# Performance work log

Measured on AMD Instinct MI355X. Metric: run time of the kernel, lower is better.

## Reference

```python
import jax, jax.numpy as jnp
import numpy as np

WIN = 7
K1 = 0.01
K2 = 0.03
COV_NORM = WIN * WIN / (WIN * WIN - 1.0)  # unbiased covariance correction


def _box_filter(t):
    # t: [B, 1, H, W]; valid conv with uniform 7x7 window (mean filter)
    w = jnp.ones((1, 1, WIN, WIN), t.dtype) / (WIN * WIN)
    return jax.lax.conv_general_dilated(
        t, w, window_strides=(1, 1), padding='VALID',
        dimension_numbers=('NCHW', 'OIHW', 'NCHW'))


def setup_inputs() -> dict:
    key = jax.random.key(0)
    kx, ky = jax.random.split(key)
    B, C, H, W = 64, 1, 384, 384
    X = jax.random.normal(kx, (B, C, H, W), dtype=jnp.float32)
    Y = jax.random.normal(ky, (B, C, H, W), dtype=jnp.float32)
    data_range = jnp.ones((B,), dtype=jnp.float32)
    return {"X": X, "Y": Y, "data_range": data_range}


def reference(X, Y, data_range):
    ux = _box_filter(X)
    uy = _box_filter(Y)
    uxx = _box_filter(X * X)
    uxy = _box_filter(X * Y)
    uyy = _box_filter(Y * Y)

    vx = COV_NORM * (uxx - ux * ux)
    vy = COV_NORM * (uyy - uy * uy)
    vxy = COV_NORM * (uxy - ux * uy)

    L = data_range.reshape(-1, 1, 1, 1)  # per-sample dynamic range
    C1 = (K1 * L) ** 2
    C2 = (K2 * L) ** 2

    N1 = 2.0 * ux * uy + C1
    N2 = 2.0 * vxy + C2
    D1 = ux * ux + uy * uy + C1
    D2 = vx + vy + C2
    S = (N1 * N2) / (D1 * D2)

    # original: mean SSIM per sample, then mean over batch; equal-size maps so
    # this equals the mean over the per-sample means
    per_sample = jnp.mean(S, axis=(1, 2, 3))
    return 1.0 - jnp.mean(per_sample)
```

## Files before the change

kernel.cpp:

```cpp
#include <hip/hip_runtime.h>

#define IMH 384
#define IMW 384
#define OH 378
#define OW 378
#define NB 64
#define SROWS 21
#define INROWS 27
#define NSTRIP 18
#define BLOCK 256
#define GSTRIDE 26
#define RING 6


template <int CTRL>
__device__ __forceinline__ float dpp_sh(float v) {
    return __int_as_float(__builtin_amdgcn_update_dpp(
        0, __float_as_int(v), CTRL, 0xf, 0xf, true));
}

__device__ __forceinline__ float2 f2add(float2 a, float2 b) { return make_float2(a.x + b.x, a.y + b.y); }
__device__ __forceinline__ float2 f2sub(float2 a, float2 b) { return make_float2(a.x - b.x, a.y - b.y); }
__device__ __forceinline__ float2 f2mul(float2 a, float2 b) { return make_float2(a.x * b.x, a.y * b.y); }
__device__ __forceinline__ float2 f2fma(float2 a, float2 b, float2 c) {
    return make_float2(fmaf(a.x, b.x, c.x), fmaf(a.y, b.y, c.y));
}
__device__ __forceinline__ float2 f2fnma(float2 a, float2 b, float2 c) {
    return make_float2(fmaf(-a.x, b.x, c.x), fmaf(-a.y, b.y, c.y));
}
__device__ __forceinline__ float2 f2fms(float2 a, float s, float2 c) {
    return make_float2(fmaf(a.x, s, -c.x), fmaf(a.y, s, -c.y));
}
__device__ __forceinline__ float2 f2s(float s) { return make_float2(s, s); }

__global__ __launch_bounds__(BLOCK)
__attribute__((amdgpu_waves_per_eu(5, 8)))
void ssim_kernel(
    const float* __restrict__ X, const float* __restrict__ Y,
    const float* __restrict__ data_range, float* __restrict__ partials)
{
    const int tid   = threadIdx.x;
    const int g     = tid >> 4;
    const int j     = tid & 15;
    const int strip = blockIdx.x;
    const int b     = blockIdx.y;
    const int y0    = strip * SROWS;

    const float* __restrict__ Xb = X + b * (IMH * IMW);
    const float* __restrict__ Yb = Y + b * (IMH * IMW);

    __shared__ float sX[RING][IMW];
    __shared__ float sY[RING][IMW];

    const bool stg = (tid < 192);
    const int  sc  = ((tid < 96) ? tid : tid - 96) * 4;
    const float* __restrict__ gp =
        ((tid < 96) ? Xb : Yb) + y0 * IMW + sc;
    float* const sbase = (tid < 96) ? &sX[0][0] : &sY[0][0];

    const int ce  = g * GSTRIDE + 2 * j;
    const int cin = min(ce, IMW - 2);
    const float2 vmask = make_float2(
        ((j <= 12) && (ce     < OW)) ? 1.f : 0.f,
        ((j <= 12) && (ce + 1 < OW)) ? 1.f : 0.f);

    const float L     = data_range[b];
    const float C1    = (0.01f * L) * (0.01f * L);
    const float C2    = (0.03f * L) * (0.03f * L);
    const float inv49 = 1.0f / 49.0f;
    const float covn  = 49.0f / 48.0f;

    if (stg) {
        #pragma unroll
        for (int k = 0; k < 5; ++k) {
            const float4 v = *(const float4*)(gp + k * IMW);
            *(float4*)(sbase + k * IMW + sc) = v;
        }
    }
    float4 gb0, gb1, gb2;
    if (stg) {
        gb0 = *(const float4*)(gp + 5 * IMW);
        gb1 = *(const float4*)(gp + 6 * IMW);
        gb2 = *(const float4*)(gp + 7 * IMW);
    }
    __syncthreads();

    float2 xh[7], yh[7];
    #pragma unroll
    for (int k = 0; k < 7; ++k) { xh[k] = f2s(0.f); yh[k] = f2s(0.f); }
    float2 V0 = f2s(0.f), V1 = f2s(0.f), V2 = f2s(0.f),
           V3 = f2s(0.f), V4 = f2s(0.f);
    float2 ls2 = f2s(0.f);

    #pragma unroll
    for (int r = 0; r < INROWS; ++r) {
        if (r + 5 < INROWS) {
            if (stg) {
                const float4 v = (r % 3 == 0) ? gb0 : (r % 3 == 1) ? gb1 : gb2;
                *(float4*)(sbase + ((r + 5) % RING) * IMW + sc) = v;
            }
        }
        if (r + 8 < INROWS) {
            if (stg) {
                const float4 v = *(const float4*)(gp + (r + 8) * IMW);
                if (r % 3 == 0) gb0 = v; else if (r % 3 == 1) gb1 = v; else gb2 = v;
            }
        }

        const float2 x = *(const float2*)&sX[r % RING][cin];
        const float2 y = *(const float2*)&sY[r % RING][cin];

        const int ks = r % 7;
        const float2 xo = xh[ks], yo = yh[ks];
        V0 = f2add(V0, f2sub(x, xo));
        V1 = f2add(V1, f2sub(y, yo));
        V2 = f2fma(x, x, V2);  V2 = f2fnma(xo, xo, V2);
        V3 = f2fma(x, y, V3);  V3 = f2fnma(xo, yo, V3);
        V4 = f2fma(y, y, V4);  V4 = f2fnma(yo, yo, V4);
        xh[ks] = x; yh[ks] = y;

        if (r >= 6) {
            const float2 Vv[5] = {V0, V1, V2, V3, V4};
            float Se[5], So[5];
            #pragma unroll
            for (int p = 0; p < 5; ++p) {
                const float e  = Vv[p].x;
                const float o  = Vv[p].y;
                const float pp = e + o;
                float B = pp + dpp_sh<0x101>(pp);
                float C = B + dpp_sh<0x102>(B);
                Se[p] = C - dpp_sh<0x103>(o);
                So[p] = C - e;
            }
            const float2 S0 = make_float2(Se[0], So[0]);
            const float2 S1 = make_float2(Se[1], So[1]);
            const float2 S2 = make_float2(Se[2], So[2]);
            const float2 S3 = make_float2(Se[3], So[3]);
            const float2 S4 = make_float2(Se[4], So[4]);

            float2 ux   = f2mul(S0, f2s(inv49));
            float2 uy   = f2mul(S1, f2s(inv49));
            float2 uxux = f2mul(ux, ux);
            float2 uyuy = f2mul(uy, uy);
            float2 uxuy = f2mul(ux, uy);
            float2 vx   = f2mul(f2fms(S2, inv49, uxux), f2s(covn));
            float2 vy   = f2mul(f2fms(S4, inv49, uyuy), f2s(covn));
            float2 vxy  = f2mul(f2fms(S3, inv49, uxuy), f2s(covn));
            float2 N1   = f2fma(f2s(2.f), uxuy, f2s(C1));
            float2 N2   = f2fma(f2s(2.f), vxy, f2s(C2));
            float2 D1   = f2add(f2add(uxux, uyuy), f2s(C1));
            float2 D2   = f2add(f2add(vx, vy), f2s(C2));
            float2 num  = f2mul(N1, N2);
            float2 den  = f2mul(D1, D2);
            const float rdd = __builtin_amdgcn_rcpf(den.x * den.y);
            float2 s2 = make_float2(num.x * den.y * rdd,
                                    num.y * den.x * rdd);
            ls2 = f2fma(s2, vmask, ls2);
        }

        __syncthreads();
    }

    float lsum = ls2.x + ls2.y;
    __shared__ float red[BLOCK / 64];
    #pragma unroll
    for (int off = 32; off > 0; off >>= 1)
        lsum += __shfl_down(lsum, off, 64);
    if ((tid & 63) == 0) red[tid >> 6] = lsum;
    __syncthreads();
    if (tid == 0) {
        float bs = 0.f;
        #pragma unroll
        for (int k = 0; k < BLOCK / 64; ++k) bs += red[k];
        partials[b * NSTRIP + strip] = bs;
    }
}

__global__ void finalize_kernel(const float* __restrict__ partials,
                                float* __restrict__ out)
{
    float v = 0.f;
    #pragma unroll
    for (int k = 0; k < NSTRIP; ++k)
        v += partials[threadIdx.x + 64 * k];
    #pragma unroll
    for (int off = 32; off > 0; off >>= 1)
        v += __shfl_down(v, off, 64);
    if (threadIdx.x == 0)
        out[0] = 1.0f - v * (1.0f / (float)(NB * OH * OW));
}

extern "C" void kernel_launch(void* const* d_in, const int* in_sizes, int n_in,
                              void* d_out, int out_size, void* d_ws, size_t ws_size,
                              hipStream_t stream) {
    const float* X  = (const float*)d_in[0];
    const float* Y  = (const float*)d_in[1];
    const float* dr = (const float*)d_in[2];
    float* out = (float*)d_out;
    float* partials = (float*)d_ws;

    dim3 grid(NSTRIP, NB);
    dim3 block(BLOCK);
    ssim_kernel<<<grid, block, 0, stream>>>(X, Y, dr, partials);
    finalize_kernel<<<1, 64, 0, stream>>>(partials, out);
}
```

Before: 31.39 us.

## Stage rows with direct global-to-LDS async loads and a vmcnt wait ladder

Replaces the register-staged global->LDS copy of input rows with global_load_lds async loads that write straight into LDS. All four waves now issue the copies, into a deeper 8-slot ring with a 6-row lookahead. The per-row __syncthreads is replaced by explicit s_waitcnt vmcnt counts followed by a raw s_barrier. The aim is to cut register staging traffic and ds_write instructions and to overlap more loads with compute. The hand-written wait ladder and raw barrier depend on precise instruction counts per thread, so ordering is fragile and LDS use grows.

```diff
diff --git a/kernel.cpp b/kernel.cpp
--- a/kernel.cpp
+++ b/kernel.cpp
@@ -10,7 +10,9 @@
 #define NSTRIP 18
 #define BLOCK 256
 #define GSTRIDE 26
-#define RING 6
+#define RING 8
+#define LA 6
+#define SLOTF 512
 
 
 template <int CTRL>
@@ -32,6 +34,16 @@
     return make_float2(fmaf(a.x, s, -c.x), fmaf(a.y, s, -c.y));
 }
 __device__ __forceinline__ float2 f2s(float s) { return make_float2(s, s); }
+
+__device__ __forceinline__ void stage16(const float* g, float* l) {
+    __builtin_amdgcn_global_load_lds(
+        (const __attribute__((address_space(1))) uint32_t*)(g),
+        (__attribute__((address_space(3))) uint32_t*)(l),
+        16, 0, 0);
+}
+
+#define WAITV(n) asm volatile("s_waitcnt vmcnt(" #n ")" ::: "memory")
+#define RAWBAR() asm volatile("s_barrier" ::: "memory")
 
 __global__ __launch_bounds__(BLOCK)
 __attribute__((amdgpu_waves_per_eu(5, 8)))
@@ -46,17 +58,18 @@
     const int b     = blockIdx.y;
     const int y0    = strip * SROWS;
 
-    const float* __restrict__ Xb = X + b * (IMH * IMW);
-    const float* __restrict__ Yb = Y + b * (IMH * IMW);
-
-    __shared__ float sX[RING][IMW];
-    __shared__ float sY[RING][IMW];
-
-    const bool stg = (tid < 192);
-    const int  sc  = ((tid < 96) ? tid : tid - 96) * 4;
-    const float* __restrict__ gp =
-        ((tid < 96) ? Xb : Yb) + y0 * IMW + sc;
-    float* const sbase = (tid < 96) ? &sX[0][0] : &sY[0][0];
+    __shared__ float sX[RING][SLOTF];
+    __shared__ float sY[RING][SLOTF];
+
+    const int wv   = tid >> 6;
+    const int ln   = tid & 63;
+    const bool isX = (wv < 2);
+    const int half = wv & 1;
+    const int foff = half * 256 + ln * 4;
+    const int fcl  = min(foff, IMW - 4);
+    const float* __restrict__ gstg =
+        (isX ? X : Y) + b * (IMH * IMW) + y0 * IMW + fcl;
+    float* const lstg = (isX ? &sX[0][0] : &sY[0][0]) + foff;
 
     const int ce  = g * GSTRIDE + 2 * j;
     const int cin = min(ce, IMW - 2);
@@ -64,26 +77,18 @@
         ((j <= 12) && (ce     < OW)) ? 1.f : 0.f,
         ((j <= 12) && (ce + 1 < OW)) ? 1.f : 0.f);
 
-    const float L     = data_range[b];
-    const float C1    = (0.01f * L) * (0.01f * L);
-    const float C2    = (0.03f * L) * (0.03f * L);
+    const float L  = data_range[b];
+    const float C1 = (0.01f * L) * (0.01f * L);
+    const float C2 = (0.03f * L) * (0.03f * L);
+    asm volatile("" :: "v"(C1), "v"(C2));
+    __builtin_amdgcn_sched_barrier(0);
+
+    #pragma unroll
+    for (int k = 0; k < LA; ++k)
+        stage16(gstg + k * IMW, lstg + k * SLOTF);
+
     const float inv49 = 1.0f / 49.0f;
     const float covn  = 49.0f / 48.0f;
-
-    if (stg) {
-        #pragma unroll
-        for (int k = 0; k < 5; ++k) {
-            const float4 v = *(const float4*)(gp + k * IMW);
-            *(float4*)(sbase + k * IMW + sc) = v;
-        }
-    }
-    float4 gb0, gb1, gb2;
-    if (stg) {
-        gb0 = *(const float4*)(gp + 5 * IMW);
-        gb1 = *(const float4*)(gp + 6 * IMW);
-        gb2 = *(const float4*)(gp + 7 * IMW);
-    }
-    __syncthreads();
 
     float2 xh[7], yh[7];
     #pragma unroll
@@ -92,20 +97,21 @@
            V3 = f2s(0.f), V4 = f2s(0.f);
     float2 ls2 = f2s(0.f);
 
+    static_assert(INROWS == 27 && LA == 6 && RING == 8, "wait ladder");
+
     #pragma unroll
     for (int r = 0; r < INROWS; ++r) {
-        if (r + 5 < INROWS) {
-            if (stg) {
-                const float4 v = (r % 3 == 0) ? gb0 : (r % 3 == 1) ? gb1 : gb2;
-                *(float4*)(sbase + ((r + 5) % RING) * IMW + sc) = v;
-            }
-        }
-        if (r + 8 < INROWS) {
-            if (stg) {
-                const float4 v = *(const float4*)(gp + (r + 8) * IMW);
-                if (r % 3 == 0) gb0 = v; else if (r % 3 == 1) gb1 = v; else gb2 = v;
-            }
-        }
+        if (r + LA < INROWS)
+            stage16(gstg + (r + LA) * IMW, lstg + ((r + LA) % RING) * SLOTF);
+
+        if      (r < 21) WAITV(6);
+        else if (r == 21) WAITV(5);
+        else if (r == 22) WAITV(4);
+        else if (r == 23) WAITV(3);
+        else if (r == 24) WAITV(2);
+        else if (r == 25) WAITV(1);
+        else              WAITV(0);
+        RAWBAR();
 
         const float2 x = *(const float2*)&sX[r % RING][cin];
         const float2 y = *(const float2*)&sY[r % RING][cin];
@@ -157,22 +163,18 @@
                                     num.y * den.x * rdd);
             ls2 = f2fma(s2, vmask, ls2);
         }
-
-        __syncthreads();
     }
 
     float lsum = ls2.x + ls2.y;
-    __shared__ float red[BLOCK / 64];
     #pragma unroll
     for (int off = 32; off > 0; off >>= 1)
         lsum += __shfl_down(lsum, off, 64);
-    if ((tid & 63) == 0) red[tid >> 6] = lsum;
+    __syncthreads();
+    if ((tid & 63) == 0) sX[0][tid >> 6] = lsum;
     __syncthreads();
     if (tid == 0) {
-        float bs = 0.f;
-        #pragma unroll
-        for (int k = 0; k < BLOCK / 64; ++k) bs += red[k];
-        partials[b * NSTRIP + strip] = bs;
+        partials[b * NSTRIP + strip] =
+            sX[0][0] + sX[0][1] + sX[0][2] + sX[0][3];
     }
 }
 
```

New measurement: 28.20 us. -10.2%, faster.
